# Kernel tuning notes

Hardware: AMD Instinct MI355X
Metric: run time of the kernel (lower is better)

## Reference

```python
import jax, jax.numpy as jnp
import numpy as np

EMBED_DIM = 64
NUM_EMB = 8192


def _conv2d(x, w, b, stride=2, pad=1):
    # x: [B,C,H,W], w: [O,I,kh,kw] -> NCHW conv, stride 2, pad 1
    y = jax.lax.conv_general_dilated(
        x, w, window_strides=(stride, stride),
        padding=[(pad, pad), (pad, pad)],
        dimension_numbers=("NCHW", "OIHW", "NCHW"))
    return y + b[None, :, None, None]


def setup_inputs() -> dict:
    key = jax.random.key(0)
    ks = jax.random.split(key, 8)
    x = jax.random.normal(ks[0], (16, 3, 256, 256), dtype=jnp.float32)
    # Kaiming-ish small init for conv params
    w1 = jax.random.normal(ks[1], (32, 3, 4, 4), dtype=jnp.float32) * 0.1
    b1 = jnp.zeros((32,), dtype=jnp.float32)
    w2 = jax.random.normal(ks[2], (64, 32, 4, 4), dtype=jnp.float32) * 0.05
    b2 = jnp.zeros((64,), dtype=jnp.float32)
    w3 = jax.random.normal(ks[3], (EMBED_DIM, 64, 4, 4), dtype=jnp.float32) * 0.05
    b3 = jnp.zeros((EMBED_DIM,), dtype=jnp.float32)
    # codebook init uniform(-1/K, 1/K) as in torch module
    codebook = jax.random.uniform(ks[4], (NUM_EMB, EMBED_DIM), dtype=jnp.float32,
                                  minval=-1.0 / NUM_EMB, maxval=1.0 / NUM_EMB)
    return {"x": x, "w1": w1, "b1": b1, "w2": w2, "b2": b2,
            "w3": w3, "b3": b3, "codebook": codebook}


def reference(x, w1, b1, w2, b2, w3, b3, codebook):
    h = jax.nn.relu(_conv2d(x, w1, b1))
    h = jax.nn.relu(_conv2d(h, w2, b2))
    z = jax.nn.relu(_conv2d(h, w3, b3))          # [B, D, 32, 32]
    z_cl = jnp.transpose(z, (0, 2, 3, 1))        # [B, 32, 32, D]
    flat = z_cl.reshape(-1, EMBED_DIM)           # [N, D]
    dists = (jnp.sum(flat * flat, axis=1, keepdims=True)
             + jnp.sum(codebook * codebook, axis=1)
             - 2.0 * jnp.matmul(flat, codebook.T))  # [N, K]
    idx = jnp.argmin(dists, axis=1)              # [N]
    idx = idx.reshape(x.shape[0], -1)            # [B, 1024]
    return idx, jnp.float32(0.0)
```

## Files before the change

### kernel.cpp

```cpp
#include <hip/hip_runtime.h>
#include <float.h>


#define TAU_ACC 2e-6f

typedef __attribute__((ext_vector_type(8))) short s16x8;
typedef __attribute__((ext_vector_type(4))) float f32x4;
typedef unsigned short ushort_t;
typedef unsigned long long u64;

static __device__ __forceinline__ unsigned short f2bf(float f) {
    unsigned u = __float_as_uint(f);
    u = (u + 0x7fffu + ((u >> 16) & 1u)) >> 16;
    return (unsigned short)u;
}
static __device__ __forceinline__ float bf2f(unsigned short h) {
    return __uint_as_float(((unsigned)h) << 16);
}

__global__ __launch_bounds__(256) void conv1_kernel(const float* __restrict__ in,
                                                    const float* __restrict__ w,
                                                    const float* __restrict__ bias,
                                                    float* __restrict__ out) {
    int p = blockIdx.x * 256 + threadIdx.x;
    int ow = p & 127, oh = (p >> 7) & 127, bb = p >> 14;
    int oc0 = blockIdx.y * 16;
    float taps[48];
    for (int ic = 0; ic < 3; ++ic) {
        const float* ip = in + (bb * 3 + ic) * 65536;
        #pragma unroll
        for (int kh = 0; kh < 4; ++kh) {
            int ih = oh * 2 - 1 + kh;
            #pragma unroll
            for (int kw = 0; kw < 4; ++kw) {
                int iw = ow * 2 - 1 + kw;
                bool ok = ((unsigned)ih < 256u) && ((unsigned)iw < 256u);
                taps[ic * 16 + kh * 4 + kw] = ok ? ip[ih * 256 + iw] : 0.0f;
            }
        }
    }
    float* op = out + bb * (32 * 16384) + oh * 128 + ow;
    for (int oc = oc0; oc < oc0 + 16; ++oc) {
        float acc = 0.0f;
        const float* wp = w + oc * 48;
        #pragma unroll
        for (int t = 0; t < 48; ++t) acc = __fmaf_rn(taps[t], wp[t], acc);
        acc = __fadd_rn(acc, bias[oc]);
        op[oc * 16384] = fmaxf(acc, 0.0f);
    }
}

__global__ __launch_bounds__(256, 4) void conv2_kernel(const float* __restrict__ in,
                                                       const float* __restrict__ w,
                                                       const float* __restrict__ bias,
                                                       float* __restrict__ out) {
    int p = blockIdx.x * 256 + threadIdx.x;
    int ow = p & 63, oh = (p >> 6) & 63, bb = p >> 12;
    int oc0 = blockIdx.y * 16;
    float acc[16];
    #pragma unroll
    for (int j = 0; j < 16; ++j) acc[j] = 0.0f;
    const float* ibase = in + bb * 32 * 16384;

    float r0[4], r1[4];
    #pragma unroll
    for (int kh = 0; kh < 4; ++kh) {
        int ih = oh * 2 - 1 + kh;
        float v0 = 0.0f, v1 = 0.0f;
        if ((unsigned)ih < 128u) {
            float2 t = *(const float2*)(ibase + ih * 128 + 2 * ow);
            v0 = t.x; v1 = t.y;
        }
        r0[kh] = v0; r1[kh] = v1;
    }
    for (int ic = 0; ic < 32; ++ic) {
        float n0[4], n1[4];
        int icn = (ic < 31) ? ic + 1 : 31;
        const float* ipn = ibase + icn * 16384;
        #pragma unroll
        for (int kh = 0; kh < 4; ++kh) {
            int ih = oh * 2 - 1 + kh;
            float v0 = 0.0f, v1 = 0.0f;
            if ((unsigned)ih < 128u) {
                float2 t = *(const float2*)(ipn + ih * 128 + 2 * ow);
                v0 = t.x; v1 = t.y;
            }
            n0[kh] = v0; n1[kh] = v1;
        }
        const float* wic = w + ic * 16;
        #pragma unroll
        for (int kh = 0; kh < 4; ++kh) {
            float t0 = __shfl_up(r1[kh], 1);
            if (ow == 0) t0 = 0.0f;
            float t3 = __shfl_down(r0[kh], 1);
            if (ow == 63) t3 = 0.0f;
            #pragma unroll
            for (int j = 0; j < 16; ++j) {
                const float* wj = wic + (oc0 + j) * 512 + kh * 4;
                acc[j] = __fmaf_rn(t0,     wj[0], acc[j]);
                acc[j] = __fmaf_rn(r0[kh], wj[1], acc[j]);
                acc[j] = __fmaf_rn(r1[kh], wj[2], acc[j]);
                acc[j] = __fmaf_rn(t3,     wj[3], acc[j]);
            }
        }
        #pragma unroll
        for (int kh = 0; kh < 4; ++kh) { r0[kh] = n0[kh]; r1[kh] = n1[kh]; }
    }
    float* op = out + bb * (64 * 4096) + oh * 64 + ow;
    #pragma unroll
    for (int j = 0; j < 16; ++j) {
        float y = __fadd_rn(acc[j], bias[oc0 + j]);
        op[(oc0 + j) * 4096] = fmaxf(y, 0.0f);
    }
}

__global__ __launch_bounds__(256) void conv3_kernel(const float* __restrict__ in,
                                                    const float* __restrict__ w,
                                                    const float* __restrict__ bias,
                                                    float* __restrict__ flat) {
    int p = blockIdx.x * 256 + threadIdx.x;
    int ow = p & 31, oh = (p >> 5) & 31, bb = p >> 10;
    int oc0 = blockIdx.y * 4;
    float acc[4];
    #pragma unroll
    for (int j = 0; j < 4; ++j) acc[j] = 0.0f;
    const float* ibase = in + bb * 64 * 4096;

    float r0[4], r1[4];
    #pragma unroll
    for (int kh = 0; kh < 4; ++kh) {
        int ih = oh * 2 - 1 + kh;
        float v0 = 0.0f, v1 = 0.0f;
        if ((unsigned)ih < 64u) {
            float2 t = *(const float2*)(ibase + ih * 64 + 2 * ow);
            v0 = t.x; v1 = t.y;
        }
        r0[kh] = v0; r1[kh] = v1;
    }
    for (int ic = 0; ic < 64; ++ic) {
        float n0[4], n1[4];
        int icn = (ic < 63) ? ic + 1 : 63;
        const float* ipn = ibase + icn * 4096;
        #pragma unroll
        for (int kh = 0; kh < 4; ++kh) {
            int ih = oh * 2 - 1 + kh;
            float v0 = 0.0f, v1 = 0.0f;
            if ((unsigned)ih < 64u) {
                float2 t = *(const float2*)(ipn + ih * 64 + 2 * ow);
                v0 = t.x; v1 = t.y;
            }
            n0[kh] = v0; n1[kh] = v1;
        }
        const float* wic = w + ic * 16;
        #pragma unroll
        for (int kh = 0; kh < 4; ++kh) {
            float t0 = __shfl_up(r1[kh], 1);
            if (ow == 0) t0 = 0.0f;
            float t3 = __shfl_down(r0[kh], 1);
            if (ow == 31) t3 = 0.0f;
            const float* wk = wic + kh * 4;
            #pragma unroll
            for (int j = 0; j < 4; ++j) acc[j] = __fmaf_rn(t0,     wk[(oc0 + j) * 1024 + 0], acc[j]);
            #pragma unroll
            for (int j = 0; j < 4; ++j) acc[j] = __fmaf_rn(r0[kh], wk[(oc0 + j) * 1024 + 1], acc[j]);
            #pragma unroll
            for (int j = 0; j < 4; ++j) acc[j] = __fmaf_rn(r1[kh], wk[(oc0 + j) * 1024 + 2], acc[j]);
            #pragma unroll
            for (int j = 0; j < 4; ++j) acc[j] = __fmaf_rn(t3,     wk[(oc0 + j) * 1024 + 3], acc[j]);
        }
        #pragma unroll
        for (int kh = 0; kh < 4; ++kh) { r0[kh] = n0[kh]; r1[kh] = n1[kh]; }
    }
    float* op = flat + (size_t)p * 64 + oc0;
    #pragma unroll
    for (int j = 0; j < 4; ++j) {
        float y = __fadd_rn(acc[j], bias[oc0 + j]);
        op[j] = fmaxf(y, 0.0f);
    }
}

__global__ __launch_bounds__(256) void rownorm_kernel(const float* __restrict__ flat,
                                                      const float* __restrict__ cb,
                                                      float* __restrict__ sx,
                                                      float* __restrict__ sc) {
    int i = blockIdx.x * 256 + threadIdx.x;
    const float* src;
    float* dst;
    if (i < 16384) { src = flat + (size_t)i * 64; dst = sx + i; }
    else           { src = cb + (size_t)(i - 16384) * 64; dst = sc + (i - 16384); }
    float r[8];
    #pragma unroll
    for (int j = 0; j < 8; ++j) r[j] = __fmul_rn(src[j], src[j]);
    #pragma unroll
    for (int b = 1; b < 8; ++b)
        #pragma unroll
        for (int j = 0; j < 8; ++j)
            r[j] = __fadd_rn(r[j], __fmul_rn(src[b * 8 + j], src[b * 8 + j]));
    float s01 = __fadd_rn(r[0], r[1]), s23 = __fadd_rn(r[2], r[3]);
    float s45 = __fadd_rn(r[4], r[5]), s67 = __fadd_rn(r[6], r[7]);
    *dst = __fadd_rn(__fadd_rn(s01, s23), __fadd_rn(s45, s67));
}

__global__ __launch_bounds__(256) void split_kernel(const float* __restrict__ flat,
                                                    const float* __restrict__ cb,
                                                    ushort_t* __restrict__ xh,
                                                    ushort_t* __restrict__ xl,
                                                    ushort_t* __restrict__ ch,
                                                    ushort_t* __restrict__ cl,
                                                    int* __restrict__ count,
                                                    float* __restrict__ out) {
    int i = blockIdx.x * 256 + threadIdx.x;
    if (i == 0) { *count = 0; out[16384] = 0.0f; }
    float v;
    ushort_t *ph, *pl;
    if (i < 1048576) { v = flat[i]; ph = xh + i; pl = xl + i; }
    else             { int j = i - 1048576; v = cb[j]; ph = ch + j; pl = cl + j; }
    unsigned short h = f2bf(v);
    unsigned short l = f2bf(v - bf2f(h));
    *ph = h; *pl = l;
}

#define SCREEN_LOAD(BH0, BH1, BL0, BL1, SCV, COL)                         \
    {                                                                     \
        size_t br_ = (size_t)(COL) * 64 + lk * 8;                         \
        BH0 = *(const s16x8*)(ch + br_);                                  \
        BH1 = *(const s16x8*)(ch + br_ + 32);                             \
        BL0 = *(const s16x8*)(cl + br_);                                  \
        BL1 = *(const s16x8*)(cl + br_ + 32);                             \
        SCV = sc[COL];                                                    \
    }

#define SCREEN_COMPUTE(BH0, BH1, BL0, BL1, SCV, COL)                      \
    {                                                                     \
        float ini_ = __fmul_rn(-0.5f, SCV);                               \
        f32x4 acc[4];                                                     \
        _Pragma("unroll")                                                 \
        for (int i = 0; i < 4; ++i) acc[i] = (f32x4){ini_, ini_, ini_, ini_}; \
        _Pragma("unroll")                                                 \
        for (int i = 0; i < 4; ++i) acc[i] = __builtin_amdgcn_mfma_f32_16x16x32_bf16(a[i][0], BH0, acc[i], 0, 0, 0); \
        _Pragma("unroll")                                                 \
        for (int i = 0; i < 4; ++i) acc[i] = __builtin_amdgcn_mfma_f32_16x16x32_bf16(a[i][1], BH1, acc[i], 0, 0, 0); \
        _Pragma("unroll")                                                 \
        for (int i = 0; i < 4; ++i) acc[i] = __builtin_amdgcn_mfma_f32_16x16x32_bf16(a[i][0], BL0, acc[i], 0, 0, 0); \
        _Pragma("unroll")                                                 \
        for (int i = 0; i < 4; ++i) acc[i] = __builtin_amdgcn_mfma_f32_16x16x32_bf16(a[i][1], BL1, acc[i], 0, 0, 0); \
        _Pragma("unroll")                                                 \
        for (int i = 0; i < 4; ++i) acc[i] = __builtin_amdgcn_mfma_f32_16x16x32_bf16(a[i][2], BH0, acc[i], 0, 0, 0); \
        _Pragma("unroll")                                                 \
        for (int i = 0; i < 4; ++i) acc[i] = __builtin_amdgcn_mfma_f32_16x16x32_bf16(a[i][3], BH1, acc[i], 0, 0, 0); \
        _Pragma("unroll")                                                 \
        for (int i = 0; i < 4; ++i) {                                     \
            _Pragma("unroll")                                             \
            for (int reg = 0; reg < 4; ++reg) {                           \
                int s_ = i * 4 + reg;                                     \
                float av_ = acc[i][reg];                                  \
                m2[s_] = __builtin_amdgcn_fmed3f(m1[s_], m2[s_], av_);    \
                i1[s_] = (av_ > m1[s_]) ? (COL) : i1[s_];                 \
                m1[s_] = fmaxf(m1[s_], av_);                              \
            }                                                             \
        }                                                                 \
    }

__global__ __launch_bounds__(512, 2) void vq_screen_kernel(const ushort_t* __restrict__ xh,
                                                           const ushort_t* __restrict__ xl,
                                                           const ushort_t* __restrict__ ch,
                                                           const ushort_t* __restrict__ cl,
                                                           const float* __restrict__ sc,
                                                           float* __restrict__ pm1,
                                                           int* __restrict__ pi1,
                                                           float* __restrict__ pm2) {
    __shared__ float lm1[8][64];
    __shared__ int   li1[8][64];
    __shared__ float lm2[8][64];
    int tid = threadIdx.x;
    int row0 = blockIdx.x * 64;
    int half = blockIdx.y;
    int kbase = half * 4096;
    int w = tid >> 6, lane = tid & 63;
    int le = lane & 15, lk = lane >> 4;

    s16x8 a[4][4];
    #pragma unroll
    for (int i = 0; i < 4; ++i) {
        size_t ar = (size_t)(row0 + i * 16 + le) * 64 + lk * 8;
        a[i][0] = *(const s16x8*)(xh + ar);
        a[i][1] = *(const s16x8*)(xh + ar + 32);
        a[i][2] = *(const s16x8*)(xl + ar);
        a[i][3] = *(const s16x8*)(xl + ar + 32);
    }

    float m1[16], m2[16];
    int i1[16];
    #pragma unroll
    for (int s = 0; s < 16; ++s) { m1[s] = -FLT_MAX; m2[s] = -FLT_MAX; i1[s] = 0x7fffffff; }

    int colbase = kbase + w * 16 + le;

    s16x8 b0h0, b0h1, b0l0, b0l1, b1h0, b1h1, b1l0, b1l1;
    float sc0, sc1;
    SCREEN_LOAD(b0h0, b0h1, b0l0, b0l1, sc0, colbase);

    for (int nbp = 0; nbp < 16; ++nbp) {
        int colA = nbp * 256 + colbase;
        int colB = colA + 128;
        int colN = (nbp < 15) ? colA + 256 : colbase;
        SCREEN_LOAD(b1h0, b1h1, b1l0, b1l1, sc1, colB);
        SCREEN_COMPUTE(b0h0, b0h1, b0l0, b0l1, sc0, colA);
        SCREEN_LOAD(b0h0, b0h1, b0l0, b0l1, sc0, colN);
        SCREEN_COMPUTE(b1h0, b1h1, b1l0, b1l1, sc1, colB);
    }

    #pragma unroll
    for (int i = 0; i < 4; ++i) {
        #pragma unroll
        for (int reg = 0; reg < 4; ++reg) {
            int s = i * 4 + reg;
            float v1 = m1[s], v2 = m2[s];
            int ix = i1[s];
            #pragma unroll
            for (int mask = 1; mask < 16; mask <<= 1) {
                float o1 = __shfl_xor(v1, mask);
                int oi = __shfl_xor(ix, mask);
                float o2 = __shfl_xor(v2, mask);
                float n2 = fmaxf(fmaxf(v2, o2), fminf(v1, o1));
                ix = (o1 > v1) ? oi : ((o1 == v1 && oi < ix) ? oi : ix);
                v1 = fmaxf(v1, o1);
                v2 = n2;
            }
            if (le == 0) {
                int rl = i * 16 + lk * 4 + reg;
                lm1[w][rl] = v1; li1[w][rl] = ix; lm2[w][rl] = v2;
            }
        }
    }
    __syncthreads();
    if (tid < 64) {
        float M1 = -FLT_MAX, M2 = -FLT_MAX;
        int I1 = 0x7fffffff;
        #pragma unroll
        for (int ww = 0; ww < 8; ++ww) {
            float a1 = lm1[ww][tid], a2 = lm2[ww][tid];
            int ai = li1[ww][tid];
            M2 = fmaxf(fmaxf(M2, a2), fminf(M1, a1));
            if (a1 > M1 || (a1 == M1 && ai < I1)) I1 = ai;
            M1 = fmaxf(M1, a1);
        }
        size_t o = (size_t)half * 16384 + row0 + tid;
        pm1[o] = M1; pi1[o] = I1; pm2[o] = M2;
    }
}

__global__ __launch_bounds__(256) void vq_merge_kernel(const float* __restrict__ pm1,
                                                       const int* __restrict__ pi1,
                                                       const float* __restrict__ pm2,
                                                       float* __restrict__ out,
                                                       int* __restrict__ count,
                                                       int* __restrict__ list,
                                                       u64* __restrict__ qbest) {
    int row = blockIdx.x * 256 + threadIdx.x;
    float a1 = pm1[row], b1 = pm1[16384 + row];
    int ai = pi1[row], bi = pi1[16384 + row];
    float a2 = pm2[row], b2 = pm2[16384 + row];
    float M1 = fmaxf(a1, b1);
    int I1 = (b1 > a1) ? bi : ai;
    float M2 = fmaxf(fmaxf(a2, b2), fminf(a1, b1));
    if (M1 - M2 >= TAU_ACC) {
        out[row] = (float)I1;
    } else {
        qbest[row] = 0xFFFFFFFFFFFFFFFFull;
        int pos = atomicAdd(count, 1);
        list[pos] = row;
    }
}

#define FLDP 68
__global__ __launch_bounds__(256) void vq_fix_kernel(const float* __restrict__ flat,
                                                     const float* __restrict__ cb,
                                                     const float* __restrict__ sx,
                                                     const float* __restrict__ sc,
                                                     const int* __restrict__ count,
                                                     const int* __restrict__ list,
                                                     u64* __restrict__ qbest) {
    __shared__ float xs[64 * FLDP];
    __shared__ float cs[128 * FLDP];
    __shared__ float sxs[64], scs[128];
    __shared__ int rowids[64];
    int n = *count;
    int rb = blockIdx.x;
    if (rb * 64 >= n) return;
    int nrows = n - rb * 64; if (nrows > 64) nrows = 64;
    int cb0 = blockIdx.y * 128;
    int tid = threadIdx.x;

    #pragma unroll
    for (int s = 0; s < 4; ++s) {
        int idx = tid + 256 * s;
        int r = idx >> 4, c = idx & 15;
        int rr = rb * 64 + r; if (rr >= n) rr = n - 1;
        int row = list[rr];
        if (c == 0) { rowids[r] = row; sxs[r] = sx[row]; }
        *(float4*)&xs[r * FLDP + c * 4] = *(const float4*)(flat + (size_t)row * 64 + c * 4);
    }
    #pragma unroll
    for (int s = 0; s < 8; ++s) {
        int idx = tid + 256 * s;
        int r = idx >> 4, c = idx & 15;
        *(float4*)&cs[r * FLDP + c * 4] = *(const float4*)(cb + (size_t)(cb0 + r) * 64 + c * 4);
    }
    if (tid < 128) scs[tid] = sc[cb0 + tid];
    __syncthreads();

    int tr = tid >> 4, tc = tid & 15;
    float acc[4][8];
    #pragma unroll
    for (int i = 0; i < 4; ++i)
        #pragma unroll
        for (int j = 0; j < 8; ++j) acc[i][j] = 0.0f;

    for (int d = 0; d < 64; d += 4) {
        float4 ax[4], bc[8];
        #pragma unroll
        for (int i = 0; i < 4; ++i) ax[i] = *(const float4*)&xs[(tr + 16 * i) * FLDP + d];
        #pragma unroll
        for (int j = 0; j < 8; ++j) bc[j] = *(const float4*)&cs[(tc + 16 * j) * FLDP + d];
        #pragma unroll
        for (int i = 0; i < 4; ++i)
            #pragma unroll
            for (int j = 0; j < 8; ++j) {
                acc[i][j] = __fmaf_rn(ax[i].x, bc[j].x, acc[i][j]);
                acc[i][j] = __fmaf_rn(ax[i].y, bc[j].y, acc[i][j]);
                acc[i][j] = __fmaf_rn(ax[i].z, bc[j].z, acc[i][j]);
                acc[i][j] = __fmaf_rn(ax[i].w, bc[j].w, acc[i][j]);
            }
    }

    float best[4];
    int bidx[4];
    #pragma unroll
    for (int i = 0; i < 4; ++i) { best[i] = FLT_MAX; bidx[i] = 0x7fffffff; }
    #pragma unroll
    for (int j = 0; j < 8; ++j) {
        int k = cb0 + tc + 16 * j;
        float scj = scs[tc + 16 * j];
        #pragma unroll
        for (int i = 0; i < 4; ++i) {
            float t1 = __fadd_rn(sxs[tr + 16 * i], scj);
            float q = __fmaf_rn(-2.0f, acc[i][j], t1);
            if (q < best[i]) { best[i] = q; bidx[i] = k; }
        }
    }

    __syncthreads();
    float* rmin = cs;
    int* ridx = (int*)(cs + 1024);
    #pragma unroll
    for (int i = 0; i < 4; ++i) {
        rmin[(tr + 16 * i) * 16 + tc] = best[i];
        ridx[(tr + 16 * i) * 16 + tc] = bidx[i];
    }
    __syncthreads();
    if (tid < nrows) {
        float m = FLT_MAX; int mi = 0x7fffffff;
        for (int t2 = 0; t2 < 16; ++t2) {
            float v = rmin[tid * 16 + t2];
            int ix = ridx[tid * 16 + t2];
            if (v < m || (v == m && ix < mi)) { m = v; mi = ix; }
        }
        u64 key = ((u64)__float_as_uint(m) << 32) | (unsigned)mi;
        atomicMin(&qbest[rowids[tid]], key);
    }
}

__global__ __launch_bounds__(256) void vq_out_kernel(const int* __restrict__ count,
                                                     const int* __restrict__ list,
                                                     const u64* __restrict__ qbest,
                                                     float* __restrict__ out) {
    int pos = blockIdx.x * 256 + threadIdx.x;
    if (pos >= *count) return;
    int row = list[pos];
    out[row] = (float)(unsigned)(qbest[row] & 0xffffffffull);
}

extern "C" void kernel_launch(void* const* d_in, const int* in_sizes, int n_in,
                              void* d_out, int out_size, void* d_ws, size_t ws_size,
                              hipStream_t stream) {
    const float* x  = (const float*)d_in[0];
    const float* w1 = (const float*)d_in[1];
    const float* b1 = (const float*)d_in[2];
    const float* w2 = (const float*)d_in[3];
    const float* b2 = (const float*)d_in[4];
    const float* w3 = (const float*)d_in[5];
    const float* b3 = (const float*)d_in[6];
    const float* cb = (const float*)d_in[7];

    float* ws   = (float*)d_ws;
    float* out1 = ws;
    ushort_t* xh = (ushort_t*)(ws + 0);
    ushort_t* xl = (ushort_t*)(ws + 524288);
    ushort_t* ch = (ushort_t*)(ws + 1048576);
    ushort_t* cl = (ushort_t*)(ws + 1310720);
    float* pm1  = ws + 1572864;
    int*   pi1  = (int*)(ws + 1605632);
    float* pm2  = ws + 1638400;
    float* out2 = ws + 8388608;
    float* flat = ws + 12582912;
    float* sx   = ws + 13631488;
    float* sc   = ws + 13647872;
    int*   count = (int*)(ws + 13656064);
    int*   list  = (int*)(ws + 13656320);
    u64*   qbest = (u64*)(ws + 13672704);
    float* out  = (float*)d_out;

    hipLaunchKernelGGL(conv1_kernel,  dim3(1024, 2), dim3(256), 0, stream, x, w1, b1, out1);
    hipLaunchKernelGGL(conv2_kernel,  dim3(256, 4), dim3(256), 0, stream, out1, w2, b2, out2);
    hipLaunchKernelGGL(conv3_kernel,  dim3(64, 16), dim3(256), 0, stream, out2, w3, b3, flat);
    hipLaunchKernelGGL(rownorm_kernel, dim3(96), dim3(256), 0, stream, flat, cb, sx, sc);
    hipLaunchKernelGGL(split_kernel,  dim3(6144), dim3(256), 0, stream, flat, cb, xh, xl, ch, cl, count, out);
    hipLaunchKernelGGL(vq_screen_kernel, dim3(256, 2), dim3(512), 0, stream,
                       xh, xl, ch, cl, sc, pm1, pi1, pm2);
    hipLaunchKernelGGL(vq_merge_kernel, dim3(64), dim3(256), 0, stream,
                       pm1, pi1, pm2, out, count, list, qbest);
    hipLaunchKernelGGL(vq_fix_kernel, dim3(256, 64), dim3(256), 0, stream,
                       flat, cb, sx, sc, count, list, qbest);
    hipLaunchKernelGGL(vq_out_kernel, dim3(64), dim3(256), 0, stream, count, list, qbest, out);
}
```

Before: 293.5 us.

## Repack conv weights oc-contiguous and grid-stride the VQ fix kernel

Adds a pre-pass that transposes conv2/conv3 weights into an [ic][tap][oc] layout, so each kh step reads output channels from contiguous addresses instead of strided ones. This makes the uniform weight loads easier to vectorise as scalar loads. The vq_fix kernel now launches 16 row-blocks and grid-strides over the candidate list instead of 256 blocks that mostly exit early. The cost is one extra kernel launch for the weight repack, plus less parallelism in vq_fix when the candidate list is long.

```diff
diff --git a/kernel.cpp b/kernel.cpp
--- a/kernel.cpp
+++ b/kernel.cpp
@@ -16,6 +16,23 @@
 }
 static __device__ __forceinline__ float bf2f(unsigned short h) {
     return __uint_as_float(((unsigned)h) << 16);
+}
+
+__global__ __launch_bounds__(256) void wpack_kernel(const float* __restrict__ w2,
+                                                    const float* __restrict__ w3,
+                                                    float* __restrict__ wp2,
+                                                    float* __restrict__ wp3) {
+    int i = blockIdx.x * 256 + threadIdx.x;
+    if (i < 32768) {
+        int oc = i >> 9, rem = i & 511;
+        int ic = rem >> 4, t = rem & 15;
+        wp2[(ic * 16 + t) * 64 + oc] = w2[i];
+    } else if (i < 98304) {
+        int j = i - 32768;
+        int oc = j >> 10, rem = j & 1023;
+        int ic = rem >> 4, t = rem & 15;
+        wp3[(ic * 16 + t) * 64 + oc] = w3[j];
+    }
 }
 
 __global__ __launch_bounds__(256) void conv1_kernel(const float* __restrict__ in,
@@ -51,7 +68,7 @@
 }
 
 __global__ __launch_bounds__(256, 4) void conv2_kernel(const float* __restrict__ in,
-                                                       const float* __restrict__ w,
+                                                       const float* __restrict__ wp,
                                                        const float* __restrict__ bias,
                                                        float* __restrict__ out) {
     int p = blockIdx.x * 256 + threadIdx.x;
@@ -87,20 +104,19 @@
             }
             n0[kh] = v0; n1[kh] = v1;
         }
-        const float* wic = w + ic * 16;
         #pragma unroll
         for (int kh = 0; kh < 4; ++kh) {
             float t0 = __shfl_up(r1[kh], 1);
             if (ow == 0) t0 = 0.0f;
             float t3 = __shfl_down(r0[kh], 1);
             if (ow == 63) t3 = 0.0f;
+            const float* wkh = wp + (ic * 16 + kh * 4) * 64 + oc0;
             #pragma unroll
             for (int j = 0; j < 16; ++j) {
-                const float* wj = wic + (oc0 + j) * 512 + kh * 4;
-                acc[j] = __fmaf_rn(t0,     wj[0], acc[j]);
-                acc[j] = __fmaf_rn(r0[kh], wj[1], acc[j]);
-                acc[j] = __fmaf_rn(r1[kh], wj[2], acc[j]);
-                acc[j] = __fmaf_rn(t3,     wj[3], acc[j]);
+                acc[j] = __fmaf_rn(t0,     wkh[j],       acc[j]);
+                acc[j] = __fmaf_rn(r0[kh], wkh[64 + j],  acc[j]);
+                acc[j] = __fmaf_rn(r1[kh], wkh[128 + j], acc[j]);
+                acc[j] = __fmaf_rn(t3,     wkh[192 + j], acc[j]);
             }
         }
         #pragma unroll
@@ -115,7 +131,7 @@
 }
 
 __global__ __launch_bounds__(256) void conv3_kernel(const float* __restrict__ in,
-                                                    const float* __restrict__ w,
+                                                    const float* __restrict__ wp,
                                                     const float* __restrict__ bias,
                                                     float* __restrict__ flat) {
     int p = blockIdx.x * 256 + threadIdx.x;
@@ -151,22 +167,21 @@
             }
             n0[kh] = v0; n1[kh] = v1;
         }
-        const float* wic = w + ic * 16;
         #pragma unroll
         for (int kh = 0; kh < 4; ++kh) {
             float t0 = __shfl_up(r1[kh], 1);
             if (ow == 0) t0 = 0.0f;
             float t3 = __shfl_down(r0[kh], 1);
             if (ow == 31) t3 = 0.0f;
-            const float* wk = wic + kh * 4;
-            #pragma unroll
-            for (int j = 0; j < 4; ++j) acc[j] = __fmaf_rn(t0,     wk[(oc0 + j) * 1024 + 0], acc[j]);
-            #pragma unroll
-            for (int j = 0; j < 4; ++j) acc[j] = __fmaf_rn(r0[kh], wk[(oc0 + j) * 1024 + 1], acc[j]);
-            #pragma unroll
-            for (int j = 0; j < 4; ++j) acc[j] = __fmaf_rn(r1[kh], wk[(oc0 + j) * 1024 + 2], acc[j]);
-            #pragma unroll
-            for (int j = 0; j < 4; ++j) acc[j] = __fmaf_rn(t3,     wk[(oc0 + j) * 1024 + 3], acc[j]);
+            const float* wkh = wp + (ic * 16 + kh * 4) * 64 + oc0;
+            #pragma unroll
+            for (int j = 0; j < 4; ++j) acc[j] = __fmaf_rn(t0,     wkh[j],       acc[j]);
+            #pragma unroll
+            for (int j = 0; j < 4; ++j) acc[j] = __fmaf_rn(r0[kh], wkh[64 + j],  acc[j]);
+            #pragma unroll
+            for (int j = 0; j < 4; ++j) acc[j] = __fmaf_rn(r1[kh], wkh[128 + j], acc[j]);
+            #pragma unroll
+            for (int j = 0; j < 4; ++j) acc[j] = __fmaf_rn(t3,     wkh[192 + j], acc[j]);
         }
         #pragma unroll
         for (int kh = 0; kh < 4; ++kh) { r0[kh] = n0[kh]; r1[kh] = n1[kh]; }
@@ -386,88 +401,90 @@
     __shared__ float sxs[64], scs[128];
     __shared__ int rowids[64];
     int n = *count;
-    int rb = blockIdx.x;
-    if (rb * 64 >= n) return;
-    int nrows = n - rb * 64; if (nrows > 64) nrows = 64;
     int cb0 = blockIdx.y * 128;
     int tid = threadIdx.x;
 
-    #pragma unroll
-    for (int s = 0; s < 4; ++s) {
-        int idx = tid + 256 * s;
-        int r = idx >> 4, c = idx & 15;
-        int rr = rb * 64 + r; if (rr >= n) rr = n - 1;
-        int row = list[rr];
-        if (c == 0) { rowids[r] = row; sxs[r] = sx[row]; }
-        *(float4*)&xs[r * FLDP + c * 4] = *(const float4*)(flat + (size_t)row * 64 + c * 4);
-    }
-    #pragma unroll
-    for (int s = 0; s < 8; ++s) {
-        int idx = tid + 256 * s;
-        int r = idx >> 4, c = idx & 15;
-        *(float4*)&cs[r * FLDP + c * 4] = *(const float4*)(cb + (size_t)(cb0 + r) * 64 + c * 4);
-    }
-    if (tid < 128) scs[tid] = sc[cb0 + tid];
-    __syncthreads();
-
-    int tr = tid >> 4, tc = tid & 15;
-    float acc[4][8];
-    #pragma unroll
-    for (int i = 0; i < 4; ++i)
-        #pragma unroll
-        for (int j = 0; j < 8; ++j) acc[i][j] = 0.0f;
-
-    for (int d = 0; d < 64; d += 4) {
-        float4 ax[4], bc[8];
-        #pragma unroll
-        for (int i = 0; i < 4; ++i) ax[i] = *(const float4*)&xs[(tr + 16 * i) * FLDP + d];
-        #pragma unroll
-        for (int j = 0; j < 8; ++j) bc[j] = *(const float4*)&cs[(tc + 16 * j) * FLDP + d];
+    for (int rb = blockIdx.x; rb * 64 < n; rb += 16) {
+        int nrows = n - rb * 64; if (nrows > 64) nrows = 64;
+
+        #pragma unroll
+        for (int s = 0; s < 4; ++s) {
+            int idx = tid + 256 * s;
+            int r = idx >> 4, c = idx & 15;
+            int rr = rb * 64 + r; if (rr >= n) rr = n - 1;
+            int row = list[rr];
+            if (c == 0) { rowids[r] = row; sxs[r] = sx[row]; }
+            *(float4*)&xs[r * FLDP + c * 4] = *(const float4*)(flat + (size_t)row * 64 + c * 4);
+        }
+        #pragma unroll
+        for (int s = 0; s < 8; ++s) {
+            int idx = tid + 256 * s;
+            int r = idx >> 4, c = idx & 15;
+            *(float4*)&cs[r * FLDP + c * 4] = *(const float4*)(cb + (size_t)(cb0 + r) * 64 + c * 4);
+        }
+        if (tid < 128) scs[tid] = sc[cb0 + tid];
+        __syncthreads();
+
+        int tr = tid >> 4, tc = tid & 15;
+        float acc[4][8];
         #pragma unroll
         for (int i = 0; i < 4; ++i)
             #pragma unroll
-            for (int j = 0; j < 8; ++j) {
-                acc[i][j] = __fmaf_rn(ax[i].x, bc[j].x, acc[i][j]);
-                acc[i][j] = __fmaf_rn(ax[i].y, bc[j].y, acc[i][j]);
-                acc[i][j] = __fmaf_rn(ax[i].z, bc[j].z, acc[i][j]);
-                acc[i][j] = __fmaf_rn(ax[i].w, bc[j].w, acc[i][j]);
-            }
-    }
-
-    float best[4];
-    int bidx[4];
-    #pragma unroll
-    for (int i = 0; i < 4; ++i) { best[i] = FLT_MAX; bidx[i] = 0x7fffffff; }
-    #pragma unroll
-    for (int j = 0; j < 8; ++j) {
-        int k = cb0 + tc + 16 * j;
-        float scj = scs[tc + 16 * j];
+            for (int j = 0; j < 8; ++j) acc[i][j] = 0.0f;
+
+        for (int d = 0; d < 64; d += 4) {
+            float4 ax[4], bc[8];
+            #pragma unroll
+            for (int i = 0; i < 4; ++i) ax[i] = *(const float4*)&xs[(tr + 16 * i) * FLDP + d];
+            #pragma unroll
+            for (int j = 0; j < 8; ++j) bc[j] = *(const float4*)&cs[(tc + 16 * j) * FLDP + d];
+            #pragma unroll
+            for (int i = 0; i < 4; ++i)
+                #pragma unroll
+                for (int j = 0; j < 8; ++j) {
+                    acc[i][j] = __fmaf_rn(ax[i].x, bc[j].x, acc[i][j]);
+                    acc[i][j] = __fmaf_rn(ax[i].y, bc[j].y, acc[i][j]);
+                    acc[i][j] = __fmaf_rn(ax[i].z, bc[j].z, acc[i][j]);
+                    acc[i][j] = __fmaf_rn(ax[i].w, bc[j].w, acc[i][j]);
+                }
+        }
+
+        float best[4];
+        int bidx[4];
+        #pragma unroll
+        for (int i = 0; i < 4; ++i) { best[i] = FLT_MAX; bidx[i] = 0x7fffffff; }
+        #pragma unroll
+        for (int j = 0; j < 8; ++j) {
+            int k = cb0 + tc + 16 * j;
+            float scj = scs[tc + 16 * j];
+            #pragma unroll
+            for (int i = 0; i < 4; ++i) {
+                float t1 = __fadd_rn(sxs[tr + 16 * i], scj);
+                float q = __fmaf_rn(-2.0f, acc[i][j], t1);
+                if (q < best[i]) { best[i] = q; bidx[i] = k; }
+            }
+        }
+
+        __syncthreads();
+        float* rmin = cs;
+        int* ridx = (int*)(cs + 1024);
         #pragma unroll
         for (int i = 0; i < 4; ++i) {
-            float t1 = __fadd_rn(sxs[tr + 16 * i], scj);
-            float q = __fmaf_rn(-2.0f, acc[i][j], t1);
-            if (q < best[i]) { best[i] = q; bidx[i] = k; }
-        }
-    }
-
-    __syncthreads();
-    float* rmin = cs;
-    int* ridx = (int*)(cs + 1024);
-    #pragma unroll
-    for (int i = 0; i < 4; ++i) {
-        rmin[(tr + 16 * i) * 16 + tc] = best[i];
-        ridx[(tr + 16 * i) * 16 + tc] = bidx[i];
-    }
-    __syncthreads();
-    if (tid < nrows) {
-        float m = FLT_MAX; int mi = 0x7fffffff;
-        for (int t2 = 0; t2 < 16; ++t2) {
-            float v = rmin[tid * 16 + t2];
-            int ix = ridx[tid * 16 + t2];
-            if (v < m || (v == m && ix < mi)) { m = v; mi = ix; }
-        }
-        u64 key = ((u64)__float_as_uint(m) << 32) | (unsigned)mi;
-        atomicMin(&qbest[rowids[tid]], key);
+            rmin[(tr + 16 * i) * 16 + tc] = best[i];
+            ridx[(tr + 16 * i) * 16 + tc] = bidx[i];
+        }
+        __syncthreads();
+        if (tid < nrows) {
+            float m = FLT_MAX; int mi = 0x7fffffff;
+            for (int t2 = 0; t2 < 16; ++t2) {
+                float v = rmin[tid * 16 + t2];
+                int ix = ridx[tid * 16 + t2];
+                if (v < m || (v == m && ix < mi)) { m = v; mi = ix; }
+            }
+            u64 key = ((u64)__float_as_uint(m) << 32) | (unsigned)mi;
+            atomicMin(&qbest[rowids[tid]], key);
+        }
+        __syncthreads();
     }
 }
 
@@ -509,18 +526,21 @@
     int*   count = (int*)(ws + 13656064);
     int*   list  = (int*)(ws + 13656320);
     u64*   qbest = (u64*)(ws + 13672704);
+    float* wp2  = ws + 13705472;
+    float* wp3  = ws + 13738240;
     float* out  = (float*)d_out;
 
+    hipLaunchKernelGGL(wpack_kernel,  dim3(384), dim3(256), 0, stream, w2, w3, wp2, wp3);
     hipLaunchKernelGGL(conv1_kernel,  dim3(1024, 2), dim3(256), 0, stream, x, w1, b1, out1);
-    hipLaunchKernelGGL(conv2_kernel,  dim3(256, 4), dim3(256), 0, stream, out1, w2, b2, out2);
-    hipLaunchKernelGGL(conv3_kernel,  dim3(64, 16), dim3(256), 0, stream, out2, w3, b3, flat);
+    hipLaunchKernelGGL(conv2_kernel,  dim3(256, 4), dim3(256), 0, stream, out1, wp2, b2, out2);
+    hipLaunchKernelGGL(conv3_kernel,  dim3(64, 16), dim3(256), 0, stream, out2, wp3, b3, flat);
     hipLaunchKernelGGL(rownorm_kernel, dim3(96), dim3(256), 0, stream, flat, cb, sx, sc);
     hipLaunchKernelGGL(split_kernel,  dim3(6144), dim3(256), 0, stream, flat, cb, xh, xl, ch, cl, count, out);
     hipLaunchKernelGGL(vq_screen_kernel, dim3(256, 2), dim3(512), 0, stream,
                        xh, xl, ch, cl, sc, pm1, pi1, pm2);
     hipLaunchKernelGGL(vq_merge_kernel, dim3(64), dim3(256), 0, stream,
                        pm1, pi1, pm2, out, count, list, qbest);
-    hipLaunchKernelGGL(vq_fix_kernel, dim3(256, 64), dim3(256), 0, stream,
+    hipLaunchKernelGGL(vq_fix_kernel, dim3(16, 64), dim3(256), 0, stream,
                        flat, cb, sx, sc, count, list, qbest);
     hipLaunchKernelGGL(vq_out_kernel, dim3(64), dim3(256), 0, stream, count, list, qbest, out);
 }
```

New measurement: 279.2 us. -4.9%, faster.
